# Kernel tuning notes

Hardware: AMD Instinct MI355X
Metric: run time of the kernel (lower is better)

## Reference

```python
import jax, jax.numpy as jnp
import numpy as np


def setup_inputs() -> dict:
    key = jax.random.key(0)
    k1, k2, k3, k4 = jax.random.split(key, 4)
    B, Cin, Cout, K, Wd, H, Wsp = 16, 256, 256, 3, 256, 64, 64
    fan_in = Cin * K * K
    return {
        "x": jax.random.normal(k1, (B, Cin, H, Wsp), dtype=jnp.float32),
        "w": jax.random.normal(k2, (B, Wd), dtype=jnp.float32),
        "conv_weight": jax.random.normal(k3, (Cout, Cin, K, K), dtype=jnp.float32) * 0.05,
        "style_w": jax.random.normal(k4, (Cin, Wd), dtype=jnp.float32) * 0.05,
        "style_b": jnp.zeros((Cin,), dtype=jnp.float32),
        "scale": jnp.asarray(1.0 / np.sqrt(fan_in), dtype=jnp.float32),
    }


def reference(x, w, conv_weight, style_w, style_b, scale):
    # x: [B, Cin, H, W]; w: [B, Wd]; conv_weight: [Cout, Cin, K, K]
    B, Cin, H, Wsp = x.shape
    Cout, _, K, _ = conv_weight.shape
    # style modulation: s = Linear(w) -> [B, 1, Cin, 1, 1]
    s = (w @ style_w.T + style_b).reshape(B, 1, Cin, 1, 1)
    # modulate + demodulate per-sample weights: [B, Cout, Cin, K, K]
    wt = (conv_weight * scale)[None] * s
    demod = jax.lax.rsqrt(jnp.sum(wt * wt, axis=(2, 3, 4), keepdims=True) + 1e-8)
    wt = (wt * demod).reshape(B * Cout, Cin, K, K)
    # grouped conv emulation: input [1, B*Cin, H, W], groups=B
    xr = x.reshape(1, B * Cin, H, Wsp)
    pad = 1
    out = jax.lax.conv_general_dilated(
        xr, wt,
        window_strides=(1, 1),
        padding=[(pad, pad), (pad, pad)],
        dimension_numbers=("NCHW", "OIHW", "NCHW"),
        feature_group_count=B,
    )
    return out.reshape(B, Cout, out.shape[2], out.shape[3])
```

## Files before the change

### kernel.cpp

```cpp
#include <hip/hip_runtime.h>
#include <hip/hip_bf16.h>

#define BB   16
#define CIN  256
#define COUT 256
#define WD   256
#define HH   64
#define WWS  64
#define NSP  4096
#define KW   9

typedef __attribute__((ext_vector_type(8))) short short8;
typedef __attribute__((ext_vector_type(4))) float f32x4;
typedef unsigned short ushort_t;
typedef unsigned int uint_t;

#define S_BYTES (BB*CIN*4)
#define WT_OFF (S_BYTES)
#define WT_BYTES (BB*9*COUT*CIN*2)
#define X_OFF (WT_OFF + WT_BYTES)
#define X_BYTES (BB*NSP*CIN*2)
#define ZP_OFF (X_OFF + X_BYTES)
#define ZP_BYTES 4096
#define WS_NEEDED ((size_t)(ZP_OFF + ZP_BYTES))

#define WAITVM4 asm volatile("s_waitcnt vmcnt(4)" ::: "memory")
#define WAITVM7 asm volatile("s_waitcnt vmcnt(7)" ::: "memory")

__device__ inline ushort_t f2bf(float f) {
    __hip_bfloat16 h = __float2bfloat16(f);
    return __builtin_bit_cast(ushort_t, h);
}

__device__ inline void gload_lds16(const ushort_t* g, ushort_t* l) {
    __builtin_amdgcn_global_load_lds(
        (const __attribute__((address_space(1))) void*)g,
        (__attribute__((address_space(3))) void*)l, 16, 0, 0);
}

__global__ __launch_bounds__(256)
void style_kernel(const float* __restrict__ w,
                  const float* __restrict__ style_w,
                  const float* __restrict__ style_b,
                  float* __restrict__ s) {
    const int b  = blockIdx.x;
    const int ci = threadIdx.x;
    __shared__ float wsh[WD];
    wsh[ci] = w[b * WD + ci];
    __syncthreads();
    const float* row = style_w + ci * WD;
    float acc = style_b[ci];
    #pragma unroll 4
    for (int k = 0; k < WD; ++k) acc += wsh[k] * row[k];
    s[b * CIN + ci] = acc;
}

__global__ __launch_bounds__(256)
void wt_kernel(const float* __restrict__ cw, const float* __restrict__ s,
               const float* __restrict__ scale_p, ushort_t* __restrict__ wt,
               float* __restrict__ zp) {
    const int co = blockIdx.x, b = blockIdx.y, ci = threadIdx.x;
    if (co == 0 && b == 0)
        ((float4*)zp)[ci] = make_float4(0.f, 0.f, 0.f, 0.f);
    const float sv = s[b * CIN + ci] * scale_p[0];
    const float* cp = cw + ((size_t)co * CIN + ci) * KW;
    float v[9];
    float ss = 0.f;
    #pragma unroll
    for (int t = 0; t < 9; ++t) { v[t] = cp[t] * sv; ss += v[t] * v[t]; }
    #pragma unroll
    for (int off = 32; off > 0; off >>= 1) ss += __shfl_down(ss, off);
    __shared__ float red[4];
    if ((ci & 63) == 0) red[ci >> 6] = ss;
    __syncthreads();
    const float dm = rsqrtf(red[0] + red[1] + red[2] + red[3] + 1e-8f);
    #pragma unroll
    for (int t = 0; t < 9; ++t)
        wt[((size_t)(b * 9 + t) * COUT + co) * CIN + ci] = f2bf(v[t] * dm);
}

__global__ __launch_bounds__(256)
void xpose_kernel(const float* __restrict__ x, ushort_t* __restrict__ xo) {
    const int spt = blockIdx.x;
    const int cit = blockIdx.y;
    const int b   = blockIdx.z;
    const int t   = threadIdx.x;
    __shared__ ushort_t tile[64 * 72];
    const int sp0 = spt * 64, ci0 = cit * 64;
    {
        const int spq = t & 15, cil = t >> 4;
        #pragma unroll
        for (int i = 0; i < 4; ++i) {
            const int ci = cil + i * 16;
            const float4 v = *(const float4*)(x + ((size_t)(b * CIN + ci0 + ci)) * NSP + sp0 + spq * 4);
            tile[(spq * 4 + 0) * 72 + ci] = f2bf(v.x);
            tile[(spq * 4 + 1) * 72 + ci] = f2bf(v.y);
            tile[(spq * 4 + 2) * 72 + ci] = f2bf(v.z);
            tile[(spq * 4 + 3) * 72 + ci] = f2bf(v.w);
        }
    }
    __syncthreads();
    {
        const int g8 = t & 7, sp = t >> 3;
        #pragma unroll
        for (int i = 0; i < 2; ++i) {
            const int spp = sp + i * 32;
            uint4 v = *(const uint4*)&tile[spp * 72 + g8 * 8];
            *(uint4*)(xo + ((size_t)(b * NSP + sp0 + spp)) * CIN + ci0 + g8 * 8) = v;
        }
    }
}

__global__ __launch_bounds__(512, 2)
void conv_mfma_kernel(const ushort_t* __restrict__ wt,
                      const ushort_t* __restrict__ xo,
                      const ushort_t* __restrict__ zp,
                      float* __restrict__ out) {
    const int wg    = blockIdx.x;
    const int b     = (wg & 7) | (((wg >> 3) & 1) << 3);
    const int ntile = wg >> 4;
    const int y0    = ntile * 4;

    const int tid  = threadIdx.x;
    const int lane = tid & 63;
    const int w    = tid >> 6;
    const int wm   = w >> 1;
    const int wn   = w & 1;
    const int wn2  = wn * 2;
    const int l15  = lane & 15;
    const int lg   = lane >> 4;
    const int lane8 = lane * 8;

    __shared__ __align__(16) ushort_t lds_a[8 * 3 * 2048];
    __shared__ __align__(16) ushort_t lds_x[2 * 6 * 66 * 32];

    const uint_t srcq8 = (uint_t)(((lane & 3) ^ (((lane >> 2) ^ (lane >> 4)) & 3)) * 8);

    const ushort_t* pa = wt + (size_t)b * (9 * COUT * CIN)
                       + (uint_t)(wm * 64 + (lane >> 2)) * CIN + srcq8;
    const int awbase = w * 6144;

    const ushort_t* px[3];
    int xdst_off[3];
    #pragma unroll
    for (int j = 0; j < 3; ++j) {
        const int cell = w * 3 + j;
        const int r    = cell >> 2;
        const int cg   = cell & 3;
        const int col  = cg * 16 + (lane >> 2);
        const int y    = y0 - 1 + r;
        const bool val = (y >= 0 && y < HH);
        px[j] = val ? (xo + (size_t)b * (NSP * CIN) + (uint_t)(y * WWS + col) * CIN + srcq8)
                    : (zp + lane8);
        xdst_off[j] = r * 2112 + (cg * 16 + 1) * 32 + lane8;
    }

    const int slotA8 = (lg ^ ((l15 ^ (l15 >> 2)) & 3)) * 8;
    int slotB8[3];
    #pragma unroll
    for (int kx = 0; kx < 3; ++kx) {
        int c2 = l15 + kx - 1;
        if (c2 < 0) c2 = 0;
        slotB8[kx] = (lg ^ ((c2 ^ (c2 >> 2)) & 3)) * 8;
    }
    const int ardbase = l15 * 32 + slotA8;

    f32x4 acc[4][8];
    #pragma unroll
    for (int mi = 0; mi < 4; ++mi)
        #pragma unroll
        for (int ni = 0; ni < 8; ++ni) acc[mi][ni] = (f32x4){0.f, 0.f, 0.f, 0.f};

    short8 af[2][4], bf[2][8];

    if (tid < 96) {
        const int cell = tid >> 2, qq = tid & 3;
        const int buf = cell / 12, cr = cell % 12;
        const int r = cr >> 1, hc = (cr & 1) * 65;
        *(uint4*)&lds_x[buf * 12672 + r * 2112 + hc * 32 + qq * 8] =
            make_uint4(0, 0, 0, 0);
    }

    #pragma unroll
    for (int j = 0; j < 3; ++j)
        gload_lds16(px[j], lds_x + xdst_off[j]);
    #pragma unroll
    for (int i = 0; i < 4; ++i)
        gload_lds16(pa + i * 4096, lds_a + awbase + i * 512 + lane8);
    #pragma unroll
    for (int i = 0; i < 4; ++i)
        gload_lds16(pa + 65536 + i * 4096, lds_a + awbase + 2048 + i * 512 + lane8);

    WAITVM4;
    asm volatile("s_waitcnt lgkmcnt(0)" ::: "memory");
    __builtin_amdgcn_sched_barrier(0);
    __builtin_amdgcn_s_barrier();

    {
        const ushort_t* ar = lds_a + awbase + ardbase;
        #pragma unroll
        for (int mi = 0; mi < 4; ++mi) af[0][mi] = *(const short8*)(ar + mi * 512);
        #pragma unroll
        for (int ni = 0; ni < 8; ++ni)
            bf[0][ni] = *(const short8*)(lds_x + (wn2 + (ni >> 2)) * 2112
                          + ((ni & 3) * 16 + l15) * 32 + slotB8[0]);
    }

    #define TAP(t, CP, cvar)                                                   \
    {                                                                          \
        constexpr int P_ = ((CP) + (t)) & 1;                                   \
        constexpr int Q_ = P_ ^ 1;                                             \
                         \
        {                                                                      \
            constexpr int tp2 = ((t) + 2) % 9;                                 \
            constexpr int bA  = ((t) + 2) % 3;                                 \
            const int ch2 = ((cvar) + (((t) + 2) / 9)) & 7;                    \
            const uint_t aoff = (uint_t)tp2 * 65536u + (uint_t)ch2 * 32u;      \
            ushort_t* ad = lds_a + awbase + bA * 2048 + lane8;                 \
            _Pragma("unroll")                                                  \
            for (int i_ = 0; i_ < 4; ++i_)                                     \
                gload_lds16(pa + aoff + i_ * 4096, ad + i_ * 512);             \
        }                                                                      \
        if ((t) == 4) {                        \
            const int cs = ((cvar) + 1) & 7;                                   \
            ushort_t* xd = lds_x + ((CP) ^ 1) * 12672;                         \
            _Pragma("unroll")                                                  \
            for (int j_ = 0; j_ < 3; ++j_)                                     \
                gload_lds16(px[j_] + cs * 32, xd + xdst_off[j_]);              \
        }                                                                      \
                \
        if ((t) == 4 || (t) == 5) { WAITVM7; } else { WAITVM4; }               \
        __builtin_amdgcn_sched_barrier(0);                                     \
                      \
        {                                                                      \
            constexpr int bA1 = ((t) + 1) % 3;                                 \
            const ushort_t* ar = lds_a + awbase + bA1 * 2048 + ardbase;        \
            _Pragma("unroll")                                                  \
            for (int mi_ = 0; mi_ < 4; ++mi_)                                  \
                af[Q_][mi_] = *(const short8*)(ar + mi_ * 512);                \
        }                                                                      \
        if ((t) < 8) {                                                         \
            constexpr int t1_ = (t) + 1;                                       \
            constexpr int ky_ = t1_ / 3, kx_ = t1_ % 3;                        \
            const ushort_t* xr = lds_x + (CP) * 12672;                         \
            _Pragma("unroll")                                                  \
            for (int ni_ = 0; ni_ < 8; ++ni_)                                  \
                bf[Q_][ni_] = *(const short8*)(xr                              \
                    + (wn2 + (ni_ >> 2) + ky_) * 2112                          \
                    + ((ni_ & 3) * 16 + l15 + kx_) * 32 + slotB8[kx_]);        \
        }                                                                      \
        __builtin_amdgcn_s_setprio(1);                                         \
        _Pragma("unroll")                                                      \
        for (int mi_ = 0; mi_ < 4; ++mi_)                                      \
            _Pragma("unroll")                                                  \
            for (int ni_ = 0; ni_ < 8; ++ni_)                                  \
                acc[mi_][ni_] = __builtin_amdgcn_mfma_f32_16x16x32_bf16(       \
                    bf[P_][ni_], af[P_][mi_], acc[mi_][ni_], 0, 0, 0);         \
        __builtin_amdgcn_s_setprio(0);                                         \
        __builtin_amdgcn_sched_barrier(0);                                     \
    }

    #define CHUNK_TAIL(CP, cvar)                                               \
    {                                                                          \
        __builtin_amdgcn_s_barrier();    \
        constexpr int Q_ = ((CP) + 9) & 1;                                     \
        const ushort_t* xr = lds_x + ((CP) ^ 1) * 12672;                       \
        _Pragma("unroll")                                                      \
        for (int ni_ = 0; ni_ < 8; ++ni_)                                      \
            bf[Q_][ni_] = *(const short8*)(xr + (wn2 + (ni_ >> 2)) * 2112      \
                + ((ni_ & 3) * 16 + l15) * 32 + slotB8[0]);                    \
    }

    #pragma unroll 1
    for (int c2 = 0; c2 < 4; ++c2) {
        const int ce = c2 * 2, cd = ce + 1;
        TAP(0, 0, ce) TAP(1, 0, ce) TAP(2, 0, ce) TAP(3, 0, ce) TAP(4, 0, ce)
        TAP(5, 0, ce) TAP(6, 0, ce) TAP(7, 0, ce) TAP(8, 0, ce)
        CHUNK_TAIL(0, ce)
        TAP(0, 1, cd) TAP(1, 1, cd) TAP(2, 1, cd) TAP(3, 1, cd) TAP(4, 1, cd)
        TAP(5, 1, cd) TAP(6, 1, cd) TAP(7, 1, cd) TAP(8, 1, cd)
        CHUNK_TAIL(1, cd)
    }
    #undef TAP
    #undef CHUNK_TAIL

    asm volatile("s_waitcnt vmcnt(0) lgkmcnt(0)" ::: "memory");
    __builtin_amdgcn_sched_barrier(0);

    #pragma unroll
    for (int mi = 0; mi < 4; ++mi) {
        const int co = wm * 64 + mi * 16 + l15;
        float* ob = out + ((size_t)(b * COUT + co)) * NSP
                  + ntile * 256 + wn * 128 + lg * 4;
        #pragma unroll
        for (int ni = 0; ni < 8; ++ni)
            *(f32x4*)(ob + (ni >> 2) * 64 + (ni & 3) * 16) = acc[mi][ni];
    }
}

__global__ __launch_bounds__(256)
void modconv_kernel(const float* __restrict__ x,
                    const float* __restrict__ cw,
                    const float* __restrict__ s,
                    const float* __restrict__ scale_p,
                    float* __restrict__ out) {
    const int tile = blockIdx.x;
    const int co   = blockIdx.y;
    const int b    = blockIdx.z;
    const int tid  = threadIdx.x;
    const float scale = scale_p[0];

    __shared__ float s_wt[CIN * KW];
    __shared__ float s_x[18 * 66];
    __shared__ float red[4];

    const float* cwb = cw + (size_t)co * CIN * KW;
    const float* sb  = s + b * CIN;
    float sumsq = 0.f;
    for (int i = tid; i < CIN * KW; i += 256) {
        float v = cwb[i] * scale * sb[i / KW];
        s_wt[i] = v;
        sumsq += v * v;
    }
    #pragma unroll
    for (int off = 32; off > 0; off >>= 1) sumsq += __shfl_down(sumsq, off);
    if ((tid & 63) == 0) red[tid >> 6] = sumsq;
    __syncthreads();
    const float demod = rsqrtf(red[0] + red[1] + red[2] + red[3] + 1e-8f);
    for (int i = tid; i < CIN * KW; i += 256) s_wt[i] *= demod;

    const int tx = tid & 63;
    const int tr = tid >> 6;
    const int y0 = tile * 16;
    float acc[4] = {0.f, 0.f, 0.f, 0.f};

    for (int ci = 0; ci < CIN; ++ci) {
        __syncthreads();
        const float* xb = x + ((size_t)(b * CIN + ci)) * (HH * WWS);
        for (int idx = tid; idx < 18 * 66; idx += 256) {
            const int r = idx / 66, c = idx % 66;
            const int yg = y0 - 1 + r, xg = c - 1;
            float v = 0.f;
            if (yg >= 0 && yg < HH && xg >= 0 && xg < WWS) v = xb[yg * WWS + xg];
            s_x[idx] = v;
        }
        __syncthreads();
        const float* wr = s_wt + ci * KW;
        const float w0 = wr[0], w1 = wr[1], w2 = wr[2];
        const float w3 = wr[3], w4 = wr[4], w5 = wr[5];
        const float w6 = wr[6], w7 = wr[7], w8 = wr[8];
        const int rbase = tr * 4;
        float xv[6][3];
        #pragma unroll
        for (int j = 0; j < 6; ++j)
            #pragma unroll
            for (int k = 0; k < 3; ++k) xv[j][k] = s_x[(rbase + j) * 66 + tx + k];
        #pragma unroll
        for (int i = 0; i < 4; ++i)
            acc[i] += w0 * xv[i][0] + w1 * xv[i][1] + w2 * xv[i][2]
                    + w3 * xv[i+1][0] + w4 * xv[i+1][1] + w5 * xv[i+1][2]
                    + w6 * xv[i+2][0] + w7 * xv[i+2][1] + w8 * xv[i+2][2];
    }
    float* ob = out + (((size_t)(b * COUT + co)) * HH + y0) * WWS + tx;
    #pragma unroll
    for (int i = 0; i < 4; ++i) ob[(tr * 4 + i) * WWS] = acc[i];
}

extern "C" void kernel_launch(void* const* d_in, const int* in_sizes, int n_in,
                              void* d_out, int out_size, void* d_ws, size_t ws_size,
                              hipStream_t stream) {
    const float* x       = (const float*)d_in[0];
    const float* w       = (const float*)d_in[1];
    const float* cw      = (const float*)d_in[2];
    const float* style_w = (const float*)d_in[3];
    const float* style_b = (const float*)d_in[4];
    const float* scale_p = (const float*)d_in[5];
    float*       out     = (float*)d_out;

    float*    s    = (float*)d_ws;
    ushort_t* wswt = (ushort_t*)((char*)d_ws + WT_OFF);
    ushort_t* wsx  = (ushort_t*)((char*)d_ws + X_OFF);
    float*    zp   = (float*)((char*)d_ws + ZP_OFF);

    style_kernel<<<dim3(BB), 256, 0, stream>>>(w, style_w, style_b, s);

    if (ws_size >= WS_NEEDED) {
        wt_kernel<<<dim3(COUT, BB), 256, 0, stream>>>(cw, s, scale_p, wswt, zp);
        xpose_kernel<<<dim3(64, 4, BB), 256, 0, stream>>>(x, wsx);
        conv_mfma_kernel<<<dim3(256), 512, 0, stream>>>(wswt, wsx,
                                                        (const ushort_t*)zp, out);
    } else {
        modconv_kernel<<<dim3(4, COUT, BB), 256, 0, stream>>>(x, cw, s, scale_p, out);
    }
}
```

Measured before the change: 112.4 us.

## Load weights directly to registers and stage half-channel x slabs in LDS

Weight fragments are now read straight from global memory into registers, two taps ahead, instead of going through a triple-buffered LDS ring. The x tile is staged in two large 128-channel halves with an XOR swizzle, replacing the per-32-channel double-buffered copies. This removes most per-chunk barriers and the LDS traffic for weights. In exchange, the kernel relies on global-load latency being hidden within two taps, and it stalls fully (vmcnt(0) plus a barrier) when switching halves.

```diff
diff --git a/kernel.cpp b/kernel.cpp
--- a/kernel.cpp
+++ b/kernel.cpp
@@ -24,8 +24,8 @@
 #define ZP_BYTES 4096
 #define WS_NEEDED ((size_t)(ZP_OFF + ZP_BYTES))
 
+#define WAITVM0 asm volatile("s_waitcnt vmcnt(0)" ::: "memory")
 #define WAITVM4 asm volatile("s_waitcnt vmcnt(4)" ::: "memory")
-#define WAITVM7 asm volatile("s_waitcnt vmcnt(7)" ::: "memory")
 
 __device__ inline ushort_t f2bf(float f) {
     __hip_bfloat16 h = __float2bfloat16(f);
@@ -129,41 +129,13 @@
     const int wn2  = wn * 2;
     const int l15  = lane & 15;
     const int lg   = lane >> 4;
-    const int lane8 = lane * 8;
-
-    __shared__ __align__(16) ushort_t lds_a[8 * 3 * 2048];
-    __shared__ __align__(16) ushort_t lds_x[2 * 6 * 66 * 32];
-
-    const uint_t srcq8 = (uint_t)(((lane & 3) ^ (((lane >> 2) ^ (lane >> 4)) & 3)) * 8);
+
+    __shared__ __align__(16) ushort_t lds_x[6 * 66 * 128];
 
     const ushort_t* pa = wt + (size_t)b * (9 * COUT * CIN)
-                       + (uint_t)(wm * 64 + (lane >> 2)) * CIN + srcq8;
-    const int awbase = w * 6144;
-
-    const ushort_t* px[3];
-    int xdst_off[3];
-    #pragma unroll
-    for (int j = 0; j < 3; ++j) {
-        const int cell = w * 3 + j;
-        const int r    = cell >> 2;
-        const int cg   = cell & 3;
-        const int col  = cg * 16 + (lane >> 2);
-        const int y    = y0 - 1 + r;
-        const bool val = (y >= 0 && y < HH);
-        px[j] = val ? (xo + (size_t)b * (NSP * CIN) + (uint_t)(y * WWS + col) * CIN + srcq8)
-                    : (zp + lane8);
-        xdst_off[j] = r * 2112 + (cg * 16 + 1) * 32 + lane8;
-    }
-
-    const int slotA8 = (lg ^ ((l15 ^ (l15 >> 2)) & 3)) * 8;
-    int slotB8[3];
-    #pragma unroll
-    for (int kx = 0; kx < 3; ++kx) {
-        int c2 = l15 + kx - 1;
-        if (c2 < 0) c2 = 0;
-        slotB8[kx] = (lg ^ ((c2 ^ (c2 >> 2)) & 3)) * 8;
-    }
-    const int ardbase = l15 * 32 + slotA8;
+                       + (uint_t)(wm * 64 + l15) * CIN + (uint_t)(lg * 8);
+
+    const ushort_t* xob = xo + (size_t)b * (NSP * CIN);
 
     f32x4 acc[4][8];
     #pragma unroll
@@ -171,118 +143,115 @@
         #pragma unroll
         for (int ni = 0; ni < 8; ++ni) acc[mi][ni] = (f32x4){0.f, 0.f, 0.f, 0.f};
 
-    short8 af[2][4], bf[2][8];
-
-    if (tid < 96) {
-        const int cell = tid >> 2, qq = tid & 3;
-        const int buf = cell / 12, cr = cell % 12;
-        const int r = cr >> 1, hc = (cr & 1) * 65;
-        *(uint4*)&lds_x[buf * 12672 + r * 2112 + hc * 32 + qq * 8] =
-            make_uint4(0, 0, 0, 0);
-    }
-
-    #pragma unroll
-    for (int j = 0; j < 3; ++j)
-        gload_lds16(px[j], lds_x + xdst_off[j]);
-    #pragma unroll
-    for (int i = 0; i < 4; ++i)
-        gload_lds16(pa + i * 4096, lds_a + awbase + i * 512 + lane8);
-    #pragma unroll
-    for (int i = 0; i < 4; ++i)
-        gload_lds16(pa + 65536 + i * 4096, lds_a + awbase + 2048 + i * 512 + lane8);
-
-    WAITVM4;
+    short8 af[2][4];
+
+    if (tid < 192) {
+        const int r = tid / 32, rem = tid % 32;
+        const int c = (rem & 1) * 65, q2 = rem >> 1;
+        *(uint4*)&lds_x[r * 8448 + c * 128 + q2 * 8] = make_uint4(0, 0, 0, 0);
+    }
+
+    #define STAGE_X(hh)                                                        \
+    {   _Pragma("unroll")                                                      \
+        for (int i_ = 0; i_ < 12; ++i_) {                                      \
+            const int id_ = w + 8 * i_;                                        \
+            const int r_  = id_ >> 4;                                \
+            const int cg_ = id_ & 15;                             \
+            const int y_  = y0 - 1 + r_;                                       \
+            const int colIdx_ = 1 + cg_ * 4 + (lane >> 4);                     \
+            const int sq_ = (lane & 15) ^ (colIdx_ & 15);                      \
+            const ushort_t* src_ = (y_ >= 0 && y_ < HH)                        \
+                ? (xob + (uint_t)(y_ * WWS + cg_ * 4 + (lane >> 4)) * CIN      \
+                       + (hh) * 128 + sq_ * 8)                                 \
+                : (zp + (lane & 15) * 8);                                      \
+            gload_lds16(src_, lds_x + r_ * 8448 + (1 + cg_ * 4) * 128          \
+                              + lane * 8);                                     \
+        }                                                                      \
+    }
+
+    STAGE_X(0);
+    #pragma unroll
+    for (int mi = 0; mi < 4; ++mi)
+        af[0][mi] = *(const short8*)(pa + mi * 4096);
+    #pragma unroll
+    for (int mi = 0; mi < 4; ++mi)
+        af[1][mi] = *(const short8*)(pa + 65536 + mi * 4096);
+
+    WAITVM0;
     asm volatile("s_waitcnt lgkmcnt(0)" ::: "memory");
     __builtin_amdgcn_sched_barrier(0);
     __builtin_amdgcn_s_barrier();
 
-    {
-        const ushort_t* ar = lds_a + awbase + ardbase;
-        #pragma unroll
-        for (int mi = 0; mi < 4; ++mi) af[0][mi] = *(const short8*)(ar + mi * 512);
-        #pragma unroll
-        for (int ni = 0; ni < 8; ++ni)
-            bf[0][ni] = *(const short8*)(lds_x + (wn2 + (ni >> 2)) * 2112
-                          + ((ni & 3) * 16 + l15) * 32 + slotB8[0]);
-    }
-
-    #define TAP(t, CP, cvar)                                                   \
+    #define TAP(t, CHPAR, cgv, xcb)                                            \
     {                                                                          \
-        constexpr int P_ = ((CP) + (t)) & 1;                                   \
-        constexpr int Q_ = P_ ^ 1;                                             \
-                         \
-        {                                                                      \
-            constexpr int tp2 = ((t) + 2) % 9;                                 \
-            constexpr int bA  = ((t) + 2) % 3;                                 \
-            const int ch2 = ((cvar) + (((t) + 2) / 9)) & 7;                    \
-            const uint_t aoff = (uint_t)tp2 * 65536u + (uint_t)ch2 * 32u;      \
-            ushort_t* ad = lds_a + awbase + bA * 2048 + lane8;                 \
-            _Pragma("unroll")                                                  \
-            for (int i_ = 0; i_ < 4; ++i_)                                     \
-                gload_lds16(pa + aoff + i_ * 4096, ad + i_ * 512);             \
-        }                                                                      \
-        if ((t) == 4) {                        \
-            const int cs = ((cvar) + 1) & 7;                                   \
-            ushort_t* xd = lds_x + ((CP) ^ 1) * 12672;                         \
-            _Pragma("unroll")                                                  \
-            for (int j_ = 0; j_ < 3; ++j_)                                     \
-                gload_lds16(px[j_] + cs * 32, xd + xdst_off[j_]);              \
-        }                                                                      \
-                \
-        if ((t) == 4 || (t) == 5) { WAITVM7; } else { WAITVM4; }               \
+        WAITVM4;                          \
         __builtin_amdgcn_sched_barrier(0);                                     \
-                      \
-        {                                                                      \
-            constexpr int bA1 = ((t) + 1) % 3;                                 \
-            const ushort_t* ar = lds_a + awbase + bA1 * 2048 + ardbase;        \
-            _Pragma("unroll")                                                  \
-            for (int mi_ = 0; mi_ < 4; ++mi_)                                  \
-                af[Q_][mi_] = *(const short8*)(ar + mi_ * 512);                \
-        }                                                                      \
-        if ((t) < 8) {                                                         \
-            constexpr int t1_ = (t) + 1;                                       \
-            constexpr int ky_ = t1_ / 3, kx_ = t1_ % 3;                        \
-            const ushort_t* xr = lds_x + (CP) * 12672;                         \
-            _Pragma("unroll")                                                  \
-            for (int ni_ = 0; ni_ < 8; ++ni_)                                  \
-                bf[Q_][ni_] = *(const short8*)(xr                              \
-                    + (wn2 + (ni_ >> 2) + ky_) * 2112                          \
-                    + ((ni_ & 3) * 16 + l15 + kx_) * 32 + slotB8[kx_]);        \
-        }                                                                      \
+        const int ky_ = (t) / 3, kx_ = (t) % 3;                                \
+        const int P_  = ((CHPAR) + (t)) & 1;                                   \
+        const ushort_t* bq_ = lds_x + (wn2 + ky_) * 8448 + xcb[kx_];           \
+        short8 bf_[8];                                                         \
+        _Pragma("unroll")                                                      \
+        for (int ni_ = 0; ni_ < 8; ++ni_)                                      \
+            bf_[ni_] = *(const short8*)(bq_ + (ni_ >> 2) * 8448                \
+                                        + (ni_ & 3) * 2048);                   \
         __builtin_amdgcn_s_setprio(1);                                         \
         _Pragma("unroll")                                                      \
         for (int mi_ = 0; mi_ < 4; ++mi_)                                      \
             _Pragma("unroll")                                                  \
             for (int ni_ = 0; ni_ < 8; ++ni_)                                  \
                 acc[mi_][ni_] = __builtin_amdgcn_mfma_f32_16x16x32_bf16(       \
-                    bf[P_][ni_], af[P_][mi_], acc[mi_][ni_], 0, 0, 0);         \
+                    bf_[ni_], af[P_][mi_], acc[mi_][ni_], 0, 0, 0);            \
         __builtin_amdgcn_s_setprio(0);                                         \
         __builtin_amdgcn_sched_barrier(0);                                     \
-    }
-
-    #define CHUNK_TAIL(CP, cvar)                                               \
-    {                                                                          \
-        __builtin_amdgcn_s_barrier();    \
-        constexpr int Q_ = ((CP) + 9) & 1;                                     \
-        const ushort_t* xr = lds_x + ((CP) ^ 1) * 12672;                       \
+        {                        \
+            const int t2_  = ((t) + 2) % 9;                                    \
+            const int cg2_ = ((cgv) + (((t) + 2) / 9)) & 7;                    \
+            const ushort_t* ap_ = pa + t2_ * 65536 + cg2_ * 32;                \
+            _Pragma("unroll")                                                  \
+            for (int mi_ = 0; mi_ < 4; ++mi_)                                  \
+                af[P_][mi_] = *(const short8*)(ap_ + mi_ * 4096);              \
+        }                                                                      \
+        __builtin_amdgcn_sched_barrier(0);                                     \
+    }
+
+    #define CHUNK9(CHPAR, cgv, clv)                                            \
+    {   int xcb[3];                                                            \
         _Pragma("unroll")                                                      \
-        for (int ni_ = 0; ni_ < 8; ++ni_)                                      \
-            bf[Q_][ni_] = *(const short8*)(xr + (wn2 + (ni_ >> 2)) * 2112      \
-                + ((ni_ & 3) * 16 + l15) * 32 + slotB8[0]);                    \
+        for (int kx_ = 0; kx_ < 3; ++kx_) {                                    \
+            const int pos_ = ((clv) * 4 + lg) ^ ((l15 + kx_) & 15);            \
+            xcb[kx_] = (l15 + kx_) * 128 + pos_ * 8;                           \
+        }                                                                      \
+        TAP(0, CHPAR, cgv, xcb) TAP(1, CHPAR, cgv, xcb)                        \
+        TAP(2, CHPAR, cgv, xcb) TAP(3, CHPAR, cgv, xcb)                        \
+        TAP(4, CHPAR, cgv, xcb) TAP(5, CHPAR, cgv, xcb)                        \
+        TAP(6, CHPAR, cgv, xcb) TAP(7, CHPAR, cgv, xcb)                        \
+        TAP(8, CHPAR, cgv, xcb)                                                \
     }
 
     #pragma unroll 1
-    for (int c2 = 0; c2 < 4; ++c2) {
-        const int ce = c2 * 2, cd = ce + 1;
-        TAP(0, 0, ce) TAP(1, 0, ce) TAP(2, 0, ce) TAP(3, 0, ce) TAP(4, 0, ce)
-        TAP(5, 0, ce) TAP(6, 0, ce) TAP(7, 0, ce) TAP(8, 0, ce)
-        CHUNK_TAIL(0, ce)
-        TAP(0, 1, cd) TAP(1, 1, cd) TAP(2, 1, cd) TAP(3, 1, cd) TAP(4, 1, cd)
-        TAP(5, 1, cd) TAP(6, 1, cd) TAP(7, 1, cd) TAP(8, 1, cd)
-        CHUNK_TAIL(1, cd)
+    for (int h = 0; h < 2; ++h) {
+        if (h) {
+            asm volatile("s_waitcnt lgkmcnt(0)" ::: "memory");
+            __builtin_amdgcn_sched_barrier(0);
+            __builtin_amdgcn_s_barrier();
+            STAGE_X(1);
+            WAITVM0;
+            __builtin_amdgcn_sched_barrier(0);
+            __builtin_amdgcn_s_barrier();
+        }
+        #pragma unroll 1
+        for (int c2 = 0; c2 < 2; ++c2) {
+            const int cl0 = c2 * 2;
+            const int cg0 = h * 4 + cl0;
+            CHUNK9(0, cg0, cl0)
+            const int cl1 = c2 * 2 + 1;
+            const int cg1 = h * 4 + cl1;
+            CHUNK9(1, cg1, cl1)
+        }
     }
     #undef TAP
-    #undef CHUNK_TAIL
+    #undef CHUNK9
+    #undef STAGE_X
 
     asm volatile("s_waitcnt vmcnt(0) lgkmcnt(0)" ::: "memory");
     __builtin_amdgcn_sched_barrier(0);
```

After: 130.3 us. 15.9% more time.
